# Performance work log

Measured on AMD Instinct MI355X. Metric: run time of the kernel, lower is better.

The kernel has to match this reference:

```python
import jax, jax.numpy as jnp
import numpy as np

B, S, D_IN, D_HID, D_OUT = 32, 512, 768, 3072, 768


def setup_inputs() -> dict:
    key = jax.random.key(0)
    k1, k2, k3, k4 = jax.random.split(key, 4)
    init_k = float(np.sqrt(1.0 / D_IN))
    init_k2 = float(np.sqrt(1.0 / D_HID))
    x = jax.random.normal(k1, (B, S, D_IN), dtype=jnp.float32)
    in_weight = jax.random.uniform(k2, (D_HID, D_IN), dtype=jnp.float32, minval=-init_k, maxval=init_k)
    in_bias = jax.random.uniform(k3, (D_HID,), dtype=jnp.float32, minval=-init_k, maxval=init_k)
    out_weight = jax.random.uniform(k4, (D_HID, D_OUT), dtype=jnp.float32, minval=-init_k2, maxval=init_k2)
    return {"x": x, "in_weight": in_weight, "in_bias": in_bias, "out_weight": out_weight}


def reference(x, in_weight, in_bias, out_weight):
    # flatten leading dims to tokens: [B*S, D_IN]
    lead = x.shape[:-1]
    xt = x.reshape(-1, in_weight.shape[1])
    # hidden = GELU(x @ W_in^T + b)   (in_weight stored [hidden, in])
    h = jax.nn.gelu(jnp.einsum('td,hd->th', xt, in_weight) + in_bias, approximate=False)
    # out = hidden @ W_out            (out_weight stored [hidden, out]; no output bias)
    out = jnp.einsum('th,ho->to', h, out_weight)
    return out.reshape(*lead, out_weight.shape[1])
```

## Files before the change

### kernel.cpp

```cpp
#include <hip/hip_runtime.h>

typedef short bf16x8 __attribute__((ext_vector_type(8)));
typedef float f32x4  __attribute__((ext_vector_type(4)));

__device__ __forceinline__ unsigned short f2bf(float f) {
    unsigned int u = __float_as_uint(f);
    u += 0x7FFFu + ((u >> 16) & 1u);
    return (unsigned short)(u >> 16);
}

__device__ __forceinline__ float gelu_f(float x) {
    float x2 = x * x;
    float u = x * (-1.5957691216f - 0.0713548162f * x2);
    float e = __expf(u);
    return x * __builtin_amdgcn_rcpf(1.0f + e);
}

__global__ void prep_all(const float* __restrict__ x,
                         const float* __restrict__ w1,
                         const float* __restrict__ w2,
                         unsigned short* __restrict__ xb,
                         unsigned short* __restrict__ w1b,
                         unsigned short* __restrict__ w2t) {
    __shared__ float tile[32][33];
    const int b = blockIdx.x, t = threadIdx.x;
    const int tx = t & 31, ty = t >> 5;
    const int o0 = (b % 24) * 32, h0 = (b / 24) * 32;
    #pragma unroll
    for (int r = 0; r < 32; r += 8)
        tile[ty + r][tx] = w2[(size_t)(h0 + ty + r) * 768 + o0 + tx];
    __syncthreads();
    #pragma unroll
    for (int r = 0; r < 32; r += 8) {
        int o = ty + r;
        w2t[(size_t)(o0 + o) * 3072 + h0 + tx] = f2bf(tile[tx][o]);
    }
    constexpr int NX = 16384 * 768 / 4, NW = 3072 * 768 / 4;
    const int stride = gridDim.x * 256;
    for (int i = b * 256 + t; i < NX + NW; i += stride) {
        const float4 v = (i < NX) ? ((const float4*)x)[i] : ((const float4*)w1)[i - NX];
        ushort4 r;
        r.x = f2bf(v.x); r.y = f2bf(v.y); r.z = f2bf(v.z); r.w = f2bf(v.w);
        if (i < NX) ((ushort4*)xb)[i] = r; else ((ushort4*)w1b)[i - NX] = r;
    }
}

template <int EPI, int K, int N, int BN>
__global__ __launch_bounds__(512, 2) void gemm_cs(
    const unsigned short* __restrict__ A,
    const unsigned short* __restrict__ B,
    const float* __restrict__ bias,
    void* __restrict__ Cp) {
    constexpr int NREP = BN / 64;
    __shared__ __align__(16) char lds[131072];
    const int t = threadIdx.x;
    const int w = t >> 6, l = t & 63;
    constexpr int ntiles = N / BN;

    int bid = blockIdx.x, nwg = gridDim.x;
    int wgid = ((nwg & 7) == 0) ? ((bid & 7) * (nwg >> 3) + (bid >> 3)) : bid;
    const int mt = wgid / ntiles, nt = wgid % ntiles;
    const int m0 = mt << 8, n0 = nt * BN;
    const int wr = w >> 2, wc = w & 3;

    const int u1 = t + 512;
    const int gu0 = (t >> 2) * K + (((t & 3) ^ ((t >> 3) & 3)) << 3);
    const int gu1 = (u1 >> 2) * K + (((u1 & 3) ^ ((u1 >> 3) & 3)) << 3);
    const unsigned short* Abase = A + (size_t)m0 * K;
    const unsigned short* Bbase = B + (size_t)n0 * K;

#define STAGE(PTR, KT, KS, REG) { \
    const unsigned short* g_ = (PTR) + (KT) * 64 + (KS) * 32; \
    __builtin_amdgcn_global_load_lds( \
        (const __attribute__((address_space(1))) void*)(g_ + gu0), \
        (__attribute__((address_space(3))) void*)(lds + (REG) + t * 16), 16, 0, 0); \
    __builtin_amdgcn_global_load_lds( \
        (const __attribute__((address_space(1))) void*)(g_ + gu1), \
        (__attribute__((address_space(3))) void*)(lds + (REG) + 8192 + t * 16), 16, 0, 0); }
#define PIN() { asm volatile("" ::: "memory"); }
#define GATE() { asm volatile("s_waitcnt vmcnt(8)\n\ts_barrier" ::: "memory"); }
#define LGKME() { asm volatile("s_waitcnt lgkmcnt(0)" ::: "memory"); }
#define RDB(RG) { const char* p_ = lds + (RG) + boffb; \
    _Pragma("unroll") \
    for (int ni_ = 0; ni_ < NREP; ++ni_) bv[ni_] = *(const bf16x8*)(p_ + ni_ * 1024); }
#define RDA(RG, MH, DST) { const char* p_ = lds + (RG) + aoffb + (MH) * 4096; \
    DST[0] = *(const bf16x8*)(p_);        DST[1] = *(const bf16x8*)(p_ + 1024); \
    DST[2] = *(const bf16x8*)(p_ + 2048); DST[3] = *(const bf16x8*)(p_ + 3072); }
#define MFMAQ(MB, AV) \
    __builtin_amdgcn_s_setprio(1); \
    _Pragma("unroll") \
    for (int mi = 0; mi < 4; ++mi) { \
        _Pragma("unroll") \
        for (int ni = 0; ni < NREP; ++ni) \
            acc[MB * 4 + mi][ni] = __builtin_amdgcn_mfma_f32_16x16x32_bf16( \
                AV[mi], bv[ni], acc[MB * 4 + mi][ni], 0, 0, 0); \
    } \
    __builtin_amdgcn_s_setprio(0);
#define PHASE(RG, SK, SS) { \
    GATE(); \
    RDB(RG); RDA(RG, 0, av); RDA(RG, 1, avh); \
    MFMAQ(0, av); MFMAQ(1, avh); \
    LGKME(); \
    STAGE(Abase, SK, SS, RG); PIN(); \
    STAGE(Bbase, SK, SS, (RG) + 32768); PIN(); }

    const int cR = l >> 4, lr = l & 15;
    const int swz = (cR ^ ((lr >> 1) & 3)) << 4;
    const int aoffb = (wr * 128 + lr) * 64 + swz;
    const int boffb = 32768 + (wc * (BN / 4) + lr) * 64 + swz;

    f32x4 acc[8][NREP];
    {
        f32x4 z = {0.f, 0.f, 0.f, 0.f};
        #pragma unroll
        for (int i = 0; i < 8; ++i)
            #pragma unroll
            for (int j = 0; j < NREP; ++j) acc[i][j] = z;
    }
    bf16x8 av[4], avh[4], bv[NREP];

    constexpr int NTK = K >> 6;
    constexpr int NT2 = K >> 7;

    STAGE(Abase, 0, 0, 0);      STAGE(Bbase, 0, 0, 32768);   PIN();
    STAGE(Abase, 0, 1, 16384);  STAGE(Bbase, 0, 1, 49152);   PIN();
    STAGE(Abase, 1, 0, 65536);  STAGE(Bbase, 1, 0, 98304);   PIN();
    STAGE(Abase, 1, 1, 81920);  STAGE(Bbase, 1, 1, 114688);  PIN();

    for (int tt = 0; tt < NT2; ++tt) {
        const int k2 = (2 * tt + 2 < NTK) ? 2 * tt + 2 : NTK - 1;
        const int k3 = (2 * tt + 3 < NTK) ? 2 * tt + 3 : NTK - 1;
        PHASE(0,     k2, 0);
        PHASE(16384, k2, 1);
        PHASE(65536, k3, 0);
        PHASE(81920, k3, 1);
    }
    asm volatile("s_waitcnt vmcnt(0)" ::: "memory");
#undef STAGE
#undef PIN
#undef GATE
#undef LGKME
#undef RDB
#undef RDA
#undef MFMAQ
#undef PHASE

    const int colb = n0 + wc * (BN / 4) + lr;
    if constexpr (EPI == 0) {
        unsigned short* Cb = (unsigned short*)Cp;
        float bvs[NREP];
        #pragma unroll
        for (int ni = 0; ni < NREP; ++ni) bvs[ni] = bias[colb + ni * 16];
        #pragma unroll
        for (int mi = 0; mi < 8; ++mi)
            #pragma unroll
            for (int j = 0; j < 4; ++j) {
                size_t row = m0 + wr * 128 + mi * 16 + cR * 4 + j;
                #pragma unroll
                for (int ni = 0; ni < NREP; ++ni) {
                    float v = acc[mi][ni][j] + bvs[ni];
                    Cb[row * N + colb + ni * 16] = f2bf(gelu_f(v));
                }
            }
    } else {
        float* Cf = (float*)Cp;
        #pragma unroll
        for (int mi = 0; mi < 8; ++mi)
            #pragma unroll
            for (int j = 0; j < 4; ++j) {
                size_t row = m0 + wr * 128 + mi * 16 + cR * 4 + j;
                #pragma unroll
                for (int ni = 0; ni < NREP; ++ni)
                    Cf[row * N + colb + ni * 16] = acc[mi][ni][j];
            }
    }
}

extern "C" void kernel_launch(void* const* d_in, const int* in_sizes, int n_in,
                              void* d_out, int out_size, void* d_ws, size_t ws_size,
                              hipStream_t stream) {
    const float* x  = (const float*)d_in[0];
    const float* w1 = (const float*)d_in[1];
    const float* b1 = (const float*)d_in[2];
    const float* w2 = (const float*)d_in[3];
    float* out = (float*)d_out;

    const int T = 16384, DIN = 768, DH = 3072, DOUT = 768;

    unsigned short* xb  = (unsigned short*)d_ws;
    unsigned short* w1b = xb  + (size_t)T * DIN;
    unsigned short* w2t = w1b + (size_t)DH * DIN;
    unsigned short* h   = w2t + (size_t)DOUT * DH;

    size_t fixed = ((size_t)T * DIN + (size_t)DH * DIN + (size_t)DOUT * DH) * 2;
    int CH = T;
    while (CH > 256 && fixed + (size_t)CH * DH * 2 > ws_size) CH >>= 1;

    prep_all<<<2304, 256, 0, stream>>>(x, w1, w2, xb, w1b, w2t);

    for (int c0 = 0; c0 < T; c0 += CH) {
        gemm_cs<0, 768, 3072, 256><<<(CH / 256) * (DH / 256), 512, 0, stream>>>(
            xb + (size_t)c0 * DIN, w1b, b1, h);
        gemm_cs<1, 3072, 768, 192><<<(CH / 256) * (DOUT / 192), 512, 0, stream>>>(
            h, w2t, b1, out + (size_t)c0 * DOUT);
    }
}
```

Before: 187.1 us.

## Double-buffer LDS fragment registers to overlap LDS reads with MFMA

Restructures the GEMM main loop into a register ping-pong. The next half-tile's A/B fragments are read from LDS into a second register set while the MFMAs on the current set run, and global-to-LDS staging is issued one full 64-wide k tile at a time. The goal is to hide LDS read latency behind matrix math instead of serialising read, compute and wait in each phase. The cost is extra VGPRs for the doubled fragments, which could spill under the 512x2 launch bounds, plus an added barrier per iteration.

```diff
diff --git a/kernel.cpp b/kernel.cpp
--- a/kernel.cpp
+++ b/kernel.cpp
@@ -46,7 +46,7 @@
 }
 
 template <int EPI, int K, int N, int BN>
-__global__ __launch_bounds__(512, 2) void gemm_cs(
+__global__ __launch_bounds__(512, 2) void gemm_rp(
     const unsigned short* __restrict__ A,
     const unsigned short* __restrict__ B,
     const float* __restrict__ bias,
@@ -79,30 +79,23 @@
         (__attribute__((address_space(3))) void*)(lds + (REG) + 8192 + t * 16), 16, 0, 0); }
 #define PIN() { asm volatile("" ::: "memory"); }
 #define GATE() { asm volatile("s_waitcnt vmcnt(8)\n\ts_barrier" ::: "memory"); }
-#define LGKME() { asm volatile("s_waitcnt lgkmcnt(0)" ::: "memory"); }
-#define RDB(RG) { const char* p_ = lds + (RG) + boffb; \
+#define LGKMB() { asm volatile("s_waitcnt lgkmcnt(0)\n\ts_barrier" ::: "memory"); }
+#define RDB(RG, BV) { const char* p_ = lds + (RG) + boffb; \
     _Pragma("unroll") \
-    for (int ni_ = 0; ni_ < NREP; ++ni_) bv[ni_] = *(const bf16x8*)(p_ + ni_ * 1024); }
+    for (int ni_ = 0; ni_ < NREP; ++ni_) BV[ni_] = *(const bf16x8*)(p_ + ni_ * 1024); }
 #define RDA(RG, MH, DST) { const char* p_ = lds + (RG) + aoffb + (MH) * 4096; \
     DST[0] = *(const bf16x8*)(p_);        DST[1] = *(const bf16x8*)(p_ + 1024); \
     DST[2] = *(const bf16x8*)(p_ + 2048); DST[3] = *(const bf16x8*)(p_ + 3072); }
-#define MFMAQ(MB, AV) \
+#define MFMAQ(MB, AV, BV) \
     __builtin_amdgcn_s_setprio(1); \
     _Pragma("unroll") \
     for (int mi = 0; mi < 4; ++mi) { \
         _Pragma("unroll") \
         for (int ni = 0; ni < NREP; ++ni) \
             acc[MB * 4 + mi][ni] = __builtin_amdgcn_mfma_f32_16x16x32_bf16( \
-                AV[mi], bv[ni], acc[MB * 4 + mi][ni], 0, 0, 0); \
+                AV[mi], BV[ni], acc[MB * 4 + mi][ni], 0, 0, 0); \
     } \
     __builtin_amdgcn_s_setprio(0);
-#define PHASE(RG, SK, SS) { \
-    GATE(); \
-    RDB(RG); RDA(RG, 0, av); RDA(RG, 1, avh); \
-    MFMAQ(0, av); MFMAQ(1, avh); \
-    LGKME(); \
-    STAGE(Abase, SK, SS, RG); PIN(); \
-    STAGE(Bbase, SK, SS, (RG) + 32768); PIN(); }
 
     const int cR = l >> 4, lr = l & 15;
     const int swz = (cR ^ ((lr >> 1) & 3)) << 4;
@@ -117,33 +110,48 @@
             #pragma unroll
             for (int j = 0; j < NREP; ++j) acc[i][j] = z;
     }
-    bf16x8 av[4], avh[4], bv[NREP];
-
-    constexpr int NTK = K >> 6;
-    constexpr int NT2 = K >> 7;
+    bf16x8 av0[4], avh0[4], bv0[NREP];
+    bf16x8 av1[4], avh1[4], bv1[NREP];
+
+    constexpr int NT = K >> 6;
 
     STAGE(Abase, 0, 0, 0);      STAGE(Bbase, 0, 0, 32768);   PIN();
     STAGE(Abase, 0, 1, 16384);  STAGE(Bbase, 0, 1, 49152);   PIN();
     STAGE(Abase, 1, 0, 65536);  STAGE(Bbase, 1, 0, 98304);   PIN();
     STAGE(Abase, 1, 1, 81920);  STAGE(Bbase, 1, 1, 114688);  PIN();
-
-    for (int tt = 0; tt < NT2; ++tt) {
-        const int k2 = (2 * tt + 2 < NTK) ? 2 * tt + 2 : NTK - 1;
-        const int k3 = (2 * tt + 3 < NTK) ? 2 * tt + 3 : NTK - 1;
-        PHASE(0,     k2, 0);
-        PHASE(16384, k2, 1);
-        PHASE(65536, k3, 0);
-        PHASE(81920, k3, 1);
+    GATE();
+    RDB(0, bv0); RDA(0, 0, av0); RDA(0, 1, avh0);
+
+    for (int kt = 0; kt < NT - 1; ++kt) {
+        const int c  = (kt & 1) << 16;
+        const int cp = 65536 - c;
+        const int k2 = (kt + 2 < NT) ? kt + 2 : NT - 1;
+        RDB(c + 16384, bv1);
+        RDA(c + 16384, 0, av1); RDA(c + 16384, 1, avh1);
+        MFMAQ(0, av0, bv0); MFMAQ(1, avh0, bv0);
+        LGKMB();
+        STAGE(Abase, k2, 0, c);          STAGE(Bbase, k2, 0, c + 32768);  PIN();
+        STAGE(Abase, k2, 1, c + 16384);  STAGE(Bbase, k2, 1, c + 49152);  PIN();
+        GATE();
+        RDB(cp, bv0); RDA(cp, 0, av0); RDA(cp, 1, avh0);
+        MFMAQ(0, av1, bv1); MFMAQ(1, avh1, bv1);
+    }
+    {
+        const int c = ((NT - 1) & 1) << 16;
+        RDB(c + 16384, bv1);
+        RDA(c + 16384, 0, av1); RDA(c + 16384, 1, avh1);
+        MFMAQ(0, av0, bv0); MFMAQ(1, avh0, bv0);
+        asm volatile("s_waitcnt lgkmcnt(0)" ::: "memory");
+        MFMAQ(0, av1, bv1); MFMAQ(1, avh1, bv1);
     }
     asm volatile("s_waitcnt vmcnt(0)" ::: "memory");
 #undef STAGE
 #undef PIN
 #undef GATE
-#undef LGKME
+#undef LGKMB
 #undef RDB
 #undef RDA
 #undef MFMAQ
-#undef PHASE
 
     const int colb = n0 + wc * (BN / 4) + lr;
     if constexpr (EPI == 0) {
@@ -199,9 +207,9 @@
     prep_all<<<2304, 256, 0, stream>>>(x, w1, w2, xb, w1b, w2t);
 
     for (int c0 = 0; c0 < T; c0 += CH) {
-        gemm_cs<0, 768, 3072, 256><<<(CH / 256) * (DH / 256), 512, 0, stream>>>(
+        gemm_rp<0, 768, 3072, 256><<<(CH / 256) * (DH / 256), 512, 0, stream>>>(
             xb + (size_t)c0 * DIN, w1b, b1, h);
-        gemm_cs<1, 3072, 768, 192><<<(CH / 256) * (DOUT / 192), 512, 0, stream>>>(
+        gemm_rp<1, 3072, 768, 192><<<(CH / 256) * (DOUT / 192), 512, 0, stream>>>(
             h, w2t, b1, out + (size_t)c0 * DOUT);
     }
 }
```

Result: slower. 207.8 us (+11.1%).
